# Kernel tuning notes

Hardware: AMD Instinct MI355X
Metric: run time of the kernel (lower is better)

## Reference

```python
import jax, jax.numpy as jnp
import numpy as np

B, FEAT, H, V = 512, 2048, 512, 100
STEPS = 200  # TEXT_MAX_LEN - 1
SOS = 0      # char2idx['<SOS>']


def setup_inputs() -> dict:
    key = jax.random.key(0)
    ks = jax.random.split(key, 8)
    s = 0.02  # small init keeps tanh/sigmoid in a sane range over 200 steps
    return {
        "feat": jax.random.normal(ks[0], (B, FEAT), jnp.float32),
        "w_hp": jax.random.normal(ks[1], (FEAT, H), jnp.float32) * s,
        "b_hp": jnp.zeros((H,), jnp.float32),
        "embed": jax.random.normal(ks[2], (V, H), jnp.float32) * s,
        "w_ih": jax.random.normal(ks[3], (3 * H, H), jnp.float32) * s,
        "w_hh": jax.random.normal(ks[4], (3 * H, H), jnp.float32) * s,
        "b_ih": jnp.zeros((3 * H,), jnp.float32),
        "b_hh": jnp.zeros((3 * H,), jnp.float32),
        "w_proj": jax.random.normal(ks[5], (H, V), jnp.float32) * s,
        "b_proj": jnp.zeros((V,), jnp.float32),
    }


def _gru_cell(x, h, w_ih, w_hh, b_ih, b_hh):
    # PyTorch GRU cell: gates ordered (reset, update, new)
    gi = x @ w_ih.T + b_ih            # [B, 3H]
    gh = h @ w_hh.T + b_hh            # [B, 3H]
    i_r, i_z, i_n = jnp.split(gi, 3, axis=-1)
    h_r, h_z, h_n = jnp.split(gh, 3, axis=-1)
    r = jax.nn.sigmoid(i_r + h_r)
    z = jax.nn.sigmoid(i_z + h_z)
    n = jnp.tanh(i_n + r * h_n)
    return (1.0 - z) * n + z * h      # new hidden = output


def reference(feat, w_hp, b_hp, embed, w_ih, w_hh, b_ih, b_hh, w_proj, b_proj):
    # hidden init = hidden_proj(resnet pooled feature)  -> [B, H]
    h0 = feat @ w_hp + b_hp
    # first input = embedding of <SOS>, broadcast over batch
    x0 = jnp.broadcast_to(embed[SOS], (feat.shape[0], embed.shape[1]))

    def step(carry, _):
        h, x = carry
        h_new = _gru_cell(x, h, w_ih, w_hh, b_ih, b_hh)
        # output feeds back as next step's input (out -> inp)
        return (h_new, h_new), h_new

    _, outs = jax.lax.scan(step, (h0, x0), None, length=STEPS)  # [T, B, H]
    res = jnp.transpose(outs, (1, 0, 2))                        # [B, T, H]
    logits = res @ w_proj + b_proj                              # [B, T, V]
    return jnp.transpose(logits, (0, 2, 1))                     # [B, V, T]
```

## Files before the change

### kernel.cpp

```cpp
#include <hip/hip_runtime.h>

#define Bsz  512
#define FEAT 2048
#define Hd   512
#define Vd   100
#define Td   200
#define Gd   2048

typedef __bf16 bf16;
typedef __bf16 bf16x8 __attribute__((ext_vector_type(8)));
typedef float  f32x4  __attribute__((ext_vector_type(4)));

__device__ bf16  g_hbuf[Td + 1][Bsz][Hd];
__device__ bf16  g_wt0[Gd][Hd];
__device__ bf16  g_wt1[Gd][Hd];
__device__ float g_bias0[Gd];
__device__ float g_bias1[Gd];
__device__ bf16  g_featbf[Bsz][FEAT];
__device__ bf16  g_whpt[Hd][FEAT];
__device__ bf16  g_wprojt[112][Hd];
__device__ float g_gi0[3 * Hd];
__device__ unsigned g_flags[8][32];
__device__ unsigned g_bar[8][32];
__device__ unsigned g_xcd[256];

template <int OFF>
__device__ __forceinline__ bf16x8 ld_b16x8_cohere(const void* p) {
  bf16x8 r;
  asm volatile("global_load_dwordx4 %0, %1, off offset:%2 sc0 sc1"
               : "=&v"(r) : "v"(p), "i"(OFF) : "memory");
  return r;
}
template <int OFF>
__device__ __forceinline__ void st_u16_cohere(void* p, unsigned short v) {
  asm volatile("global_store_short %0, %1, off offset:%2 sc0 sc1"
               :: "v"(p), "v"(v), "i"(OFF) : "memory");
}
__device__ __forceinline__ void st_u32_cohere(void* p, unsigned v) {
  asm volatile("global_store_dword %0, %1, off sc0 sc1" :: "v"(p), "v"(v) : "memory");
}
__device__ __forceinline__ unsigned ld_u32_cohere(const void* p) {
  unsigned r;
  asm volatile("global_load_dword %0, %1, off sc0 sc1\n\ts_waitcnt vmcnt(0)"
               : "=&v"(r) : "v"(p) : "memory");
  return r;
}
__device__ __forceinline__ unsigned atomic_rd_l2(unsigned* p) {
  unsigned r;
  asm volatile("global_atomic_add %0, %1, %2, off sc0\n\ts_waitcnt vmcnt(0)"
               : "=&v"(r) : "v"(p), "v"(0u) : "memory");
  return r;
}
__device__ __forceinline__ void atomic_inc_l2(unsigned* p) {
  asm volatile("global_atomic_add %0, %1, off" :: "v"(p), "v"(1u) : "memory");
}
__device__ __forceinline__ void atomic_pf(void* p) {
  asm volatile("global_atomic_add %0, %1, off" :: "v"(p), "v"(0u) : "memory");
}
__device__ __forceinline__ void wait_vm0() { asm volatile("s_waitcnt vmcnt(0)" ::: "memory"); }
__device__ __forceinline__ void wait_vm8() { asm volatile("s_waitcnt vmcnt(8)" ::: "memory"); }

#define LDA16(arr, base) do {                                                   \
  arr[0]  = ld_b16x8_cohere<0>(base);   arr[1]  = ld_b16x8_cohere<64>(base);    \
  arr[2]  = ld_b16x8_cohere<128>(base); arr[3]  = ld_b16x8_cohere<192>(base);   \
  arr[4]  = ld_b16x8_cohere<256>(base); arr[5]  = ld_b16x8_cohere<320>(base);   \
  arr[6]  = ld_b16x8_cohere<384>(base); arr[7]  = ld_b16x8_cohere<448>(base);   \
  arr[8]  = ld_b16x8_cohere<512>(base); arr[9]  = ld_b16x8_cohere<576>(base);   \
  arr[10] = ld_b16x8_cohere<640>(base); arr[11] = ld_b16x8_cohere<704>(base);   \
  arr[12] = ld_b16x8_cohere<768>(base); arr[13] = ld_b16x8_cohere<832>(base);   \
  arr[14] = ld_b16x8_cohere<896>(base); arr[15] = ld_b16x8_cohere<960>(base);   \
} while (0)

__device__ __forceinline__ float sigmoidf_(float x) {
  x = fminf(fmaxf(x, -30.f), 30.f);
  return 1.f / (1.f + __expf(-x));
}
__device__ __forceinline__ float tanhf_(float x) {
  x = fminf(fmaxf(x, -15.f), 15.f);
  float e = __expf(2.f * x);
  return (e - 1.f) / (e + 1.f);
}

__device__ __forceinline__ void group_barrier(int rg, int cg, unsigned phase) {
  wait_vm0();
  __syncthreads();
  if (threadIdx.x == 0) st_u32_cohere(&g_flags[rg][cg], phase);
  if (threadIdx.x < 64) {
    const unsigned* fp = &g_flags[rg][threadIdx.x & 31];
    while (ld_u32_cohere(fp) < phase) __builtin_amdgcn_s_sleep(1);
  }
  __syncthreads();
}

__device__ __forceinline__ void barrier_fast2(unsigned* cnt, unsigned target) {
  wait_vm0();
  __syncthreads();
  if (threadIdx.x == 0) {
    atomic_inc_l2(cnt);
    while (atomic_rd_l2(cnt) < target) __builtin_amdgcn_s_sleep(1);
  }
  __syncthreads();
}


__global__ void k_conv_feat(const float* feat) {
  int i = blockIdx.x * 256 + threadIdx.x;
  if (i < Bsz * FEAT) ((bf16*)g_featbf)[i] = (bf16)feat[i];
  if (blockIdx.x == 0) {
    ((unsigned*)g_flags)[threadIdx.x] = 0u;
    ((unsigned*)g_bar)[threadIdx.x] = 0u;
    g_xcd[threadIdx.x] = 0xffffffffu;
  }
}

__global__ void k_gi0(const float* embed, const float* w_ih, const float* b_ih) {
  int j = blockIdx.x;
  const float* wr = w_ih + (size_t)j * Hd;
  float s = 0.f;
  for (int k = threadIdx.x; k < Hd; k += 64) s += embed[k] * wr[k];
#pragma unroll
  for (int off = 32; off > 0; off >>= 1) s += __shfl_down(s, off);
  if (threadIdx.x == 0) g_gi0[j] = s + b_ih[j];
}

__global__ void k_build_wt1(const float* w_ih, const float* w_hh,
                            const float* b_ih, const float* b_hh) {
  int c = blockIdx.x;
  int j = (c >> 6) * 16 + (c & 15);
  int f = (c >> 4) & 3;
  const float* s1 = nullptr; const float* s2 = nullptr; float bias;
  if (f == 0)      { s1 = w_ih + (size_t)j * Hd;            s2 = w_hh + (size_t)j * Hd;            bias = b_ih[j] + b_hh[j]; }
  else if (f == 1) { s1 = w_ih + (size_t)(Hd + j) * Hd;     s2 = w_hh + (size_t)(Hd + j) * Hd;     bias = b_ih[Hd + j] + b_hh[Hd + j]; }
  else if (f == 2) { s1 = w_ih + (size_t)(2 * Hd + j) * Hd;                                        bias = b_ih[2 * Hd + j]; }
  else             { s1 = w_hh + (size_t)(2 * Hd + j) * Hd;                                        bias = b_hh[2 * Hd + j]; }
  for (int k = threadIdx.x; k < Hd; k += 256) {
    float v = s1[k] + (s2 ? s2[k] : 0.f);
    g_wt1[c][k] = (bf16)v;
  }
  if (threadIdx.x == 0) g_bias1[c] = bias;
}

__global__ void k_build_wt0(const float* w_hh, const float* b_hh) {
  int c = blockIdx.x;
  int j = (c >> 6) * 16 + (c & 15);
  int f = (c >> 4) & 3;
  const float* s1 = nullptr; float bias;
  if (f == 0)      { s1 = w_hh + (size_t)j * Hd;            bias = g_gi0[j] + b_hh[j]; }
  else if (f == 1) { s1 = w_hh + (size_t)(Hd + j) * Hd;     bias = g_gi0[Hd + j] + b_hh[Hd + j]; }
  else if (f == 2) {                                        bias = g_gi0[2 * Hd + j]; }
  else             { s1 = w_hh + (size_t)(2 * Hd + j) * Hd; bias = b_hh[2 * Hd + j]; }
  for (int k = threadIdx.x; k < Hd; k += 256)
    g_wt0[c][k] = (bf16)(s1 ? s1[k] : 0.f);
  if (threadIdx.x == 0) g_bias0[c] = bias;
}

__global__ void k_build_whpt(const float* w_hp) {
  int n = blockIdx.x;
  for (int k = threadIdx.x; k < FEAT; k += 256)
    g_whpt[n][k] = (bf16)w_hp[(size_t)k * Hd + n];
}

__global__ void k_build_wprojt(const float* w_proj) {
  int v = blockIdx.x;
  for (int k = threadIdx.x; k < Hd; k += 256)
    g_wprojt[v][k] = (bf16)(v < Vd ? w_proj[(size_t)k * Vd + v] : 0.f);
}

__global__ __launch_bounds__(256, 1) void k_gru_seq(const float* b_hp) {
  const int bid = blockIdx.x;
  const int rg = bid & 7;
  const int cg = bid >> 3;
  const int w = threadIdx.x >> 6, l = threadIdx.x & 63;
  const int m = l & 15;
  const int ksub = (l >> 4) * 8;
  const int colb = cg * 64;
  const int arow = rg * 64 + w * 16 + m;
  const int orow = rg * 64 + w * 16 + (l >> 4) * 4;
  const int hcol = cg * 16 + m;
  __shared__ int s_fast;

  bf16x8 Bw[64];
#pragma unroll
  for (int f = 0; f < 4; f++)
#pragma unroll
    for (int k0 = 0; k0 < 16; k0++)
      Bw[f * 16 + k0] = *(const bf16x8*)&g_wt1[colb + f * 16 + m][k0 * 32 + ksub];

  float b0v[4], b1v[4];
#pragma unroll
  for (int f = 0; f < 4; f++) {
    b0v[f] = g_bias0[colb + f * 16 + m];
    b1v[f] = g_bias1[colb + f * 16 + m];
  }

  unsigned xcc;
  asm volatile("s_getreg_b32 %0, hwreg(HW_REG_XCC_ID)" : "=s"(xcc));
  if (threadIdx.x == 0) st_u32_cohere(&g_xcd[bid], xcc);
  group_barrier(rg, cg, 1u);
  if (threadIdx.x < 64) {
    unsigned peer = ld_u32_cohere(&g_xcd[rg + 8 * (threadIdx.x & 31)]);
    unsigned long long bal = __ballot(peer == xcc);
    if (threadIdx.x == 0) s_fast = (bal == ~0ull) ? 1 : 0;
  }
  __syncthreads();
  const bool fast = (s_fast != 0);

  float hcarry[4];
  {
    f32x4 acc = {0.f, 0.f, 0.f, 0.f};
#pragma unroll 4
    for (int k0 = 0; k0 < FEAT; k0 += 32) {
      bf16x8 a = *(const bf16x8*)&g_featbf[arow][k0 + ksub];
      bf16x8 b = *(const bf16x8*)&g_whpt[hcol][k0 + ksub];
      acc = __builtin_amdgcn_mfma_f32_16x16x32_bf16(a, b, acc, 0, 0, 0);
    }
    float bhp = b_hp[hcol];
    bf16* pb = &g_hbuf[0][orow][hcol];
    unsigned short us[4];
#pragma unroll
    for (int i = 0; i < 4; i++) {
      bf16 hv = (bf16)(acc[i] + bhp);
      hcarry[i] = (float)hv;
      us[i] = __builtin_bit_cast(unsigned short, hv);
    }
    if (fast) {
#pragma unroll
      for (int i = 0; i < 4; i++) pb[i * Hd] = __builtin_bit_cast(bf16, us[i]);
    } else {
      char* pc = (char*)pb;
      st_u16_cohere<0>(pc, us[0]);    st_u16_cohere<1024>(pc, us[1]);
      st_u16_cohere<2048>(pc, us[2]); st_u16_cohere<3072>(pc, us[3]);
    }
  }

  if (fast) {
    unsigned* cnt = &g_bar[rg][0];
    barrier_fast2(cnt, 32u * 1);

    for (int t = 0; t < Td; t++) {
      bf16x8 a[16];
      const bf16* Ap = &g_hbuf[t][arow][ksub];
#pragma unroll
      for (int k0 = 0; k0 < 16; k0++) a[k0] = *(const bf16x8*)(Ap + k0 * 32);

      if (threadIdx.x < 64) atomic_pf((void*)&g_hbuf[t + 1][rg * 64 + threadIdx.x][cg * 16]);

      f32x4 acc[4], acc2[4];
#pragma unroll
      for (int f = 0; f < 4; f++) {
        float bv = (t == 0) ? b0v[f] : b1v[f];
        acc[f]  = (f32x4){bv, bv, bv, bv};
        acc2[f] = (f32x4){0.f, 0.f, 0.f, 0.f};
      }
      if (t == 0) {
#pragma unroll
        for (int k0 = 0; k0 < 8; k0++)
#pragma unroll
          for (int f = 0; f < 4; f++) {
            bf16x8 b = *(const bf16x8*)&g_wt0[colb + f * 16 + m][k0 * 32 + ksub];
            acc[f] = __builtin_amdgcn_mfma_f32_16x16x32_bf16(a[k0], b, acc[f], 0, 0, 0);
          }
#pragma unroll
        for (int k0 = 8; k0 < 16; k0++)
#pragma unroll
          for (int f = 0; f < 4; f++) {
            bf16x8 b = *(const bf16x8*)&g_wt0[colb + f * 16 + m][k0 * 32 + ksub];
            acc2[f] = __builtin_amdgcn_mfma_f32_16x16x32_bf16(a[k0], b, acc2[f], 0, 0, 0);
          }
      } else {
#pragma unroll
        for (int k0 = 0; k0 < 8; k0++)
#pragma unroll
          for (int f = 0; f < 4; f++)
            acc[f] = __builtin_amdgcn_mfma_f32_16x16x32_bf16(a[k0], Bw[f * 16 + k0], acc[f], 0, 0, 0);
#pragma unroll
        for (int k0 = 8; k0 < 16; k0++)
#pragma unroll
          for (int f = 0; f < 4; f++)
            acc2[f] = __builtin_amdgcn_mfma_f32_16x16x32_bf16(a[k0], Bw[f * 16 + k0], acc2[f], 0, 0, 0);
      }

      bf16* pb = &g_hbuf[t + 1][orow][hcol];
#pragma unroll
      for (int i = 0; i < 4; i++) {
        float r = sigmoidf_(acc[0][i] + acc2[0][i]);
        float z = sigmoidf_(acc[1][i] + acc2[1][i]);
        float n = tanhf_((acc[2][i] + acc2[2][i]) + r * (acc[3][i] + acc2[3][i]));
        float hn = (1.f - z) * n + z * hcarry[i];
        bf16 hv = (bf16)hn;
        hcarry[i] = (float)hv;
        pb[i * Hd] = hv;
      }
      if (t < Td - 1) barrier_fast2(cnt, 32u * (unsigned)(t + 2));
    }
  } else {
    group_barrier(rg, cg, 2u);
    for (int t = 0; t < Td; t++) {
      bf16x8 a[16];
      const char* Ap = (const char*)&g_hbuf[t][arow][ksub];
      LDA16(a, Ap);

      f32x4 acc[4];
#pragma unroll
      for (int f = 0; f < 4; f++) {
        float bv = (t == 0) ? b0v[f] : b1v[f];
        acc[f] = (f32x4){bv, bv, bv, bv};
      }
      if (t == 0) {
        wait_vm0(); __builtin_amdgcn_sched_barrier(0);
#pragma unroll
        for (int k0 = 0; k0 < 16; k0++)
#pragma unroll
          for (int f = 0; f < 4; f++) {
            bf16x8 b = *(const bf16x8*)&g_wt0[colb + f * 16 + m][k0 * 32 + ksub];
            acc[f] = __builtin_amdgcn_mfma_f32_16x16x32_bf16(a[k0], b, acc[f], 0, 0, 0);
          }
      } else {
        wait_vm8(); __builtin_amdgcn_sched_barrier(0);
#pragma unroll
        for (int k0 = 0; k0 < 8; k0++)
#pragma unroll
          for (int f = 0; f < 4; f++)
            acc[f] = __builtin_amdgcn_mfma_f32_16x16x32_bf16(a[k0], Bw[f * 16 + k0], acc[f], 0, 0, 0);
        wait_vm0(); __builtin_amdgcn_sched_barrier(0);
#pragma unroll
        for (int k0 = 8; k0 < 16; k0++)
#pragma unroll
          for (int f = 0; f < 4; f++)
            acc[f] = __builtin_amdgcn_mfma_f32_16x16x32_bf16(a[k0], Bw[f * 16 + k0], acc[f], 0, 0, 0);
      }

      char* pb = (char*)&g_hbuf[t + 1][orow][hcol];
      unsigned short us[4];
#pragma unroll
      for (int i = 0; i < 4; i++) {
        float r = sigmoidf_(acc[0][i]);
        float z = sigmoidf_(acc[1][i]);
        float n = tanhf_(acc[2][i] + r * acc[3][i]);
        float hn = (1.f - z) * n + z * hcarry[i];
        bf16 hv = (bf16)hn;
        hcarry[i] = (float)hv;
        us[i] = __builtin_bit_cast(unsigned short, hv);
      }
      st_u16_cohere<0>(pb, us[0]);    st_u16_cohere<1024>(pb, us[1]);
      st_u16_cohere<2048>(pb, us[2]); st_u16_cohere<3072>(pb, us[3]);

      if (t < Td - 1) group_barrier(rg, cg, (unsigned)(t + 3));
    }
  }
  wait_vm0();
}

__global__ __launch_bounds__(256) void k_proj(const float* b_proj, float* out) {
  int b = blockIdx.x;
  int w = threadIdx.x >> 6, l = threadIdx.x & 63;
  int tt = blockIdx.y * 4 + w;
  if (tt > 12) return;
  int m = l & 15, ksub = (l >> 4) * 8;
  int tcol = tt * 16 + m;
  int trow = (tcol < Td ? tcol : Td - 1) + 1;

  f32x4 acc[7];
#pragma unroll
  for (int f = 0; f < 7; f++)
#pragma unroll
    for (int i = 0; i < 4; i++) {
      int v = f * 16 + (l >> 4) * 4 + i;
      acc[f][i] = (v < Vd) ? b_proj[v] : 0.f;
    }

  bf16x8 bb[16];
  const bf16* Bp = &g_hbuf[trow][b][ksub];
#pragma unroll
  for (int k0 = 0; k0 < 16; k0++) bb[k0] = *(const bf16x8*)(Bp + k0 * 32);

#pragma unroll
  for (int k0 = 0; k0 < 16; k0++)
#pragma unroll
    for (int f = 0; f < 7; f++) {
      bf16x8 afrag = *(const bf16x8*)&g_wprojt[f * 16 + m][k0 * 32 + ksub];
      acc[f] = __builtin_amdgcn_mfma_f32_16x16x32_bf16(afrag, bb[k0], acc[f], 0, 0, 0);
    }

  if (tcol < Td) {
#pragma unroll
    for (int f = 0; f < 7; f++)
#pragma unroll
      for (int i = 0; i < 4; i++) {
        int v = f * 16 + (l >> 4) * 4 + i;
        if (v < Vd) out[((size_t)b * Vd + v) * Td + tcol] = acc[f][i];
      }
  }
}

extern "C" void kernel_launch(void* const* d_in, const int* in_sizes, int n_in,
                              void* d_out, int out_size, void* d_ws, size_t ws_size,
                              hipStream_t stream) {
  const float* feat   = (const float*)d_in[0];
  const float* w_hp   = (const float*)d_in[1];
  const float* b_hp   = (const float*)d_in[2];
  const float* embed  = (const float*)d_in[3];
  const float* w_ih   = (const float*)d_in[4];
  const float* w_hh   = (const float*)d_in[5];
  const float* b_ih   = (const float*)d_in[6];
  const float* b_hh   = (const float*)d_in[7];
  const float* w_proj = (const float*)d_in[8];
  const float* b_proj = (const float*)d_in[9];
  float* out = (float*)d_out;

  hipLaunchKernelGGL(k_conv_feat, dim3((Bsz * FEAT) / 256), dim3(256), 0, stream, feat);
  hipLaunchKernelGGL(k_gi0, dim3(3 * Hd), dim3(64), 0, stream, embed, w_ih, b_ih);
  hipLaunchKernelGGL(k_build_wt1, dim3(Gd), dim3(256), 0, stream, w_ih, w_hh, b_ih, b_hh);
  hipLaunchKernelGGL(k_build_wt0, dim3(Gd), dim3(256), 0, stream, w_hh, b_hh);
  hipLaunchKernelGGL(k_build_whpt, dim3(Hd), dim3(256), 0, stream, w_hp);
  hipLaunchKernelGGL(k_build_wprojt, dim3(112), dim3(256), 0, stream, w_proj);
  hipLaunchKernelGGL(k_gru_seq, dim3(256), dim3(256), 0, stream, b_hp);
  hipLaunchKernelGGL(k_proj, dim3(Bsz, 4), dim3(256), 0, stream, b_proj, out);
}
```

Baseline: 1.034 ms.

## Use ping-pong hidden buffer with L2 loads and split MFMA waits in fast path

Measured after the change: 1.050 ms. No clear change (+1.5%).

```diff
diff --git a/kernel.cpp b/kernel.cpp
--- a/kernel.cpp
+++ b/kernel.cpp
@@ -12,6 +12,7 @@
 typedef float  f32x4  __attribute__((ext_vector_type(4)));
 
 __device__ bf16  g_hbuf[Td + 1][Bsz][Hd];
+__device__ bf16  g_hping[2][Bsz][Hd];
 __device__ bf16  g_wt0[Gd][Hd];
 __device__ bf16  g_wt1[Gd][Hd];
 __device__ float g_bias0[Gd];
@@ -32,6 +33,13 @@
   return r;
 }
 template <int OFF>
+__device__ __forceinline__ bf16x8 ld_b16x8_l2(const void* p) {
+  bf16x8 r;
+  asm volatile("global_load_dwordx4 %0, %1, off offset:%2 sc1"
+               : "=&v"(r) : "v"(p), "i"(OFF) : "memory");
+  return r;
+}
+template <int OFF>
 __device__ __forceinline__ void st_u16_cohere(void* p, unsigned short v) {
   asm volatile("global_store_short %0, %1, off offset:%2 sc0 sc1"
                :: "v"(p), "v"(v), "i"(OFF) : "memory");
@@ -45,17 +53,14 @@
                : "=&v"(r) : "v"(p) : "memory");
   return r;
 }
-__device__ __forceinline__ unsigned atomic_rd_l2(unsigned* p) {
+__device__ __forceinline__ unsigned atomic_rd(unsigned* p) {
   unsigned r;
   asm volatile("global_atomic_add %0, %1, %2, off sc0\n\ts_waitcnt vmcnt(0)"
                : "=&v"(r) : "v"(p), "v"(0u) : "memory");
   return r;
 }
-__device__ __forceinline__ void atomic_inc_l2(unsigned* p) {
+__device__ __forceinline__ void atomic_inc(unsigned* p) {
   asm volatile("global_atomic_add %0, %1, off" :: "v"(p), "v"(1u) : "memory");
-}
-__device__ __forceinline__ void atomic_pf(void* p) {
-  asm volatile("global_atomic_add %0, %1, off" :: "v"(p), "v"(0u) : "memory");
 }
 __device__ __forceinline__ void wait_vm0() { asm volatile("s_waitcnt vmcnt(0)" ::: "memory"); }
 __device__ __forceinline__ void wait_vm8() { asm volatile("s_waitcnt vmcnt(8)" ::: "memory"); }
@@ -71,6 +76,17 @@
   arr[14] = ld_b16x8_cohere<896>(base); arr[15] = ld_b16x8_cohere<960>(base);   \
 } while (0)
 
+#define LDA16_L2(arr, base) do {                                                \
+  arr[0]  = ld_b16x8_l2<0>(base);   arr[1]  = ld_b16x8_l2<64>(base);            \
+  arr[2]  = ld_b16x8_l2<128>(base); arr[3]  = ld_b16x8_l2<192>(base);           \
+  arr[4]  = ld_b16x8_l2<256>(base); arr[5]  = ld_b16x8_l2<320>(base);           \
+  arr[6]  = ld_b16x8_l2<384>(base); arr[7]  = ld_b16x8_l2<448>(base);           \
+  arr[8]  = ld_b16x8_l2<512>(base); arr[9]  = ld_b16x8_l2<576>(base);           \
+  arr[10] = ld_b16x8_l2<640>(base); arr[11] = ld_b16x8_l2<704>(base);           \
+  arr[12] = ld_b16x8_l2<768>(base); arr[13] = ld_b16x8_l2<832>(base);           \
+  arr[14] = ld_b16x8_l2<896>(base); arr[15] = ld_b16x8_l2<960>(base);           \
+} while (0)
+
 __device__ __forceinline__ float sigmoidf_(float x) {
   x = fminf(fmaxf(x, -30.f), 30.f);
   return 1.f / (1.f + __expf(-x));
@@ -88,16 +104,6 @@
   if (threadIdx.x < 64) {
     const unsigned* fp = &g_flags[rg][threadIdx.x & 31];
     while (ld_u32_cohere(fp) < phase) __builtin_amdgcn_s_sleep(1);
-  }
-  __syncthreads();
-}
-
-__device__ __forceinline__ void barrier_fast2(unsigned* cnt, unsigned target) {
-  wait_vm0();
-  __syncthreads();
-  if (threadIdx.x == 0) {
-    atomic_inc_l2(cnt);
-    while (atomic_rd_l2(cnt) < target) __builtin_amdgcn_s_sleep(1);
   }
   __syncthreads();
 }
@@ -215,7 +221,8 @@
       acc = __builtin_amdgcn_mfma_f32_16x16x32_bf16(a, b, acc, 0, 0, 0);
     }
     float bhp = b_hp[hcol];
-    bf16* pb = &g_hbuf[0][orow][hcol];
+    bf16* ph = &g_hbuf[0][orow][hcol];
+    bf16* pp = &g_hping[0][orow][hcol];
     unsigned short us[4];
 #pragma unroll
     for (int i = 0; i < 4; i++) {
@@ -225,9 +232,12 @@
     }
     if (fast) {
 #pragma unroll
-      for (int i = 0; i < 4; i++) pb[i * Hd] = __builtin_bit_cast(bf16, us[i]);
+      for (int i = 0; i < 4; i++) {
+        pp[i * Hd] = __builtin_bit_cast(bf16, us[i]);
+        ph[i * Hd] = __builtin_bit_cast(bf16, us[i]);
+      }
     } else {
-      char* pc = (char*)pb;
+      char* pc = (char*)ph;
       st_u16_cohere<0>(pc, us[0]);    st_u16_cohere<1024>(pc, us[1]);
       st_u16_cohere<2048>(pc, us[2]); st_u16_cohere<3072>(pc, us[3]);
     }
@@ -235,15 +245,18 @@
 
   if (fast) {
     unsigned* cnt = &g_bar[rg][0];
-    barrier_fast2(cnt, 32u * 1);
+    wait_vm0();
+    __syncthreads();
+    if (threadIdx.x == 0) {
+      atomic_inc(cnt);
+      while (atomic_rd(cnt) < 32u) __builtin_amdgcn_s_sleep(1);
+    }
+    __syncthreads();
 
     for (int t = 0; t < Td; t++) {
       bf16x8 a[16];
-      const bf16* Ap = &g_hbuf[t][arow][ksub];
-#pragma unroll
-      for (int k0 = 0; k0 < 16; k0++) a[k0] = *(const bf16x8*)(Ap + k0 * 32);
-
-      if (threadIdx.x < 64) atomic_pf((void*)&g_hbuf[t + 1][rg * 64 + threadIdx.x][cg * 16]);
+      const char* Ap = (const char*)&g_hping[t & 1][arow][ksub];
+      LDA16_L2(a, Ap);
 
       f32x4 acc[4], acc2[4];
 #pragma unroll
@@ -252,6 +265,7 @@
         acc[f]  = (f32x4){bv, bv, bv, bv};
         acc2[f] = (f32x4){0.f, 0.f, 0.f, 0.f};
       }
+      wait_vm8(); __builtin_amdgcn_sched_barrier(0);
       if (t == 0) {
 #pragma unroll
         for (int k0 = 0; k0 < 8; k0++)
@@ -260,6 +274,7 @@
             bf16x8 b = *(const bf16x8*)&g_wt0[colb + f * 16 + m][k0 * 32 + ksub];
             acc[f] = __builtin_amdgcn_mfma_f32_16x16x32_bf16(a[k0], b, acc[f], 0, 0, 0);
           }
+        wait_vm0(); __builtin_amdgcn_sched_barrier(0);
 #pragma unroll
         for (int k0 = 8; k0 < 16; k0++)
 #pragma unroll
@@ -273,6 +288,7 @@
 #pragma unroll
           for (int f = 0; f < 4; f++)
             acc[f] = __builtin_amdgcn_mfma_f32_16x16x32_bf16(a[k0], Bw[f * 16 + k0], acc[f], 0, 0, 0);
+        wait_vm0(); __builtin_amdgcn_sched_barrier(0);
 #pragma unroll
         for (int k0 = 8; k0 < 16; k0++)
 #pragma unroll
@@ -280,7 +296,8 @@
             acc2[f] = __builtin_amdgcn_mfma_f32_16x16x32_bf16(a[k0], Bw[f * 16 + k0], acc2[f], 0, 0, 0);
       }
 
-      bf16* pb = &g_hbuf[t + 1][orow][hcol];
+      bf16 hv4[4];
+      bf16* pp = &g_hping[(t + 1) & 1][orow][hcol];
 #pragma unroll
       for (int i = 0; i < 4; i++) {
         float r = sigmoidf_(acc[0][i] + acc2[0][i]);
@@ -289,9 +306,24 @@
         float hn = (1.f - z) * n + z * hcarry[i];
         bf16 hv = (bf16)hn;
         hcarry[i] = (float)hv;
-        pb[i * Hd] = hv;
-      }
-      if (t < Td - 1) barrier_fast2(cnt, 32u * (unsigned)(t + 2));
+        hv4[i] = hv;
+        pp[i * Hd] = hv;
+      }
+      wait_vm0();
+
+      bf16* ph = &g_hbuf[t + 1][orow][hcol];
+#pragma unroll
+      for (int i = 0; i < 4; i++) ph[i * Hd] = hv4[i];
+
+      if (t < Td - 1) {
+        __syncthreads();
+        if (threadIdx.x == 0) {
+          atomic_inc(cnt);
+          unsigned tgt = 32u * (unsigned)(t + 2);
+          while (atomic_rd(cnt) < tgt) __builtin_amdgcn_s_sleep(1);
+        }
+        __syncthreads();
+      }
     }
   } else {
     group_barrier(rg, cg, 2u);
```
